# Kernel optimization log

Hardware: AMD Instinct MI355X
Metric: run time of the kernel (lower is better)

Reference implementation:

```python
import jax, jax.numpy as jnp
import numpy as np

DEGREE = 3
NUM_KNOTS = 64
NUM_NEURONS = 256
BATCH = 4096


def _extended_knots():
    """Replicates knots_distribution + sklearn SplineTransformer knot extension.

    Base knots (nk-2 values): linspace(-0.002,-0.001,dg) ++ linspace(0,1,nk-2*dg-2)
    ++ linspace(1.001,1.002,dg). sklearn then pads `degree` knots on each side
    using the boundary knot spacing, giving M = nk - 2 + 2*degree knots and
    M - degree - 1 = nk + degree - 3 = nk basis functions (degree==3).
    """
    dg, nk = DEGREE, NUM_KNOTS
    base = np.concatenate([
        np.linspace(-0.002, -0.001, dg),
        np.linspace(0.0, 1.0, nk - 2 * dg - 2),
        np.linspace(1.001, 1.002, dg),
    ])
    dist_lo = base[1] - base[0]
    dist_hi = base[-1] - base[-2]
    left = base[0] - dist_lo * np.arange(dg, 0, -1)
    right = base[-1] + dist_hi * np.arange(1, dg + 1)
    return jnp.asarray(np.concatenate([left, base, right]), dtype=jnp.float32)


def _bspline_basis(x, t, degree):
    """Vectorized Cox-de Boor recursion.

    x: (..., ) samples; t: (M,) extended knots.
    Returns basis of shape (..., M - degree - 1).
    """
    xe = x[..., None]
    # order-0: indicator of half-open knot intervals, shape (..., M-1)
    B = ((t[:-1] <= xe) & (xe < t[1:])).astype(x.dtype)
    for k in range(1, degree + 1):
        d1 = t[k:-1] - t[:-k - 1]   # (M-k-1,)
        d2 = t[k + 1:] - t[1:-k]    # (M-k-1,)
        w1 = jnp.where(d1 != 0, (xe - t[:-k - 1]) / jnp.where(d1 != 0, d1, 1.0), 0.0)
        w2 = jnp.where(d2 != 0, (t[k + 1:] - xe) / jnp.where(d2 != 0, d2, 1.0), 0.0)
        B = w1 * B[..., :-1] + w2 * B[..., 1:]
    return B


def setup_inputs() -> dict:
    key = jax.random.key(0)
    k1, k2, k3 = jax.random.split(key, 3)
    x = jax.random.uniform(k1, (BATCH, NUM_NEURONS), dtype=jnp.float32)
    control_p = jax.random.normal(k2, (NUM_KNOTS, NUM_NEURONS), dtype=jnp.float32)
    bias = jax.random.normal(k3, (NUM_NEURONS,), dtype=jnp.float32)
    return {"x": x, "control_p": control_p, "bias": bias}


def reference(x, control_p, bias):
    t = _extended_knots()
    # Same B-spline knot vector for every feature, so compute basis jointly:
    # basis[b, f, k] == (torch) basises.permute(1,2,0)[b, k, f]
    basis = _bspline_basis(x, t, DEGREE)          # (batch, F, num_knots)
    out = jnp.einsum('bfk,kf->bf', basis, control_p) + bias
    return out
```

## Files before the change

### kernel.cpp

```cpp
#include <hip/hip_runtime.h>

#define NF 256
#define NT 68

__device__ __forceinline__ float knotf(int idx) {
    if (idx <= 5) return -0.0035f + 0.0005f * (float)idx;
    if (idx >= 62) return 1.001f + 0.0005f * (float)(idx - 62);
    int j = idx - 6;
    if (j == 55) return 1.0f;
    return (float)((double)j * (1.0 / 55.0));
}

__global__ __launch_bounds__(256) void bspline_kernel(
    const float* __restrict__ x,
    const float* __restrict__ cp,
    const float* __restrict__ bias,
    float* __restrict__ out,
    int total4)
{
    __shared__ float t[NT];
    __shared__ float rd11[61], rd21[61], rd22[61], rd31[61], rd32[61], rd33[61];

    const int tid = threadIdx.x;
    if (tid < NT) t[tid] = knotf(tid);
    __syncthreads();
    if (tid >= 6 && tid <= 60) {
        rd11[tid] = 1.0f / (t[tid + 1] - t[tid]);
        rd21[tid] = 1.0f / (t[tid + 1] - t[tid - 1]);
        rd22[tid] = 1.0f / (t[tid + 2] - t[tid]);
        rd31[tid] = 1.0f / (t[tid + 1] - t[tid - 2]);
        rd32[tid] = 1.0f / (t[tid + 2] - t[tid - 1]);
        rd33[tid] = 1.0f / (t[tid + 3] - t[tid]);
    }
    __syncthreads();

    const int gid = blockIdx.x * blockDim.x + tid;
    if (gid >= total4) return;

    const float4 xv = reinterpret_cast<const float4*>(x)[gid];
    const int f0 = (gid * 4) & (NF - 1);
    const float4 bv = reinterpret_cast<const float4*>(bias)[f0 >> 2];

    float xs[4] = {xv.x, xv.y, xv.z, xv.w};
    float rs[4];

#pragma unroll
    for (int l = 0; l < 4; ++l) {
        const float xx = xs[l];
        int j = (int)(xx * 55.0f);
        j = j < 0 ? 0 : (j > 54 ? 54 : j);
        int i = j + 6;
        if (i > 6 && xx < t[i]) --i;
        else if (i < 60 && xx >= t[i + 1]) ++i;

        const float l1 = xx - t[i];
        const float r1 = t[i + 1] - xx;
        const float l2 = xx - t[i - 1];
        const float r2 = t[i + 2] - xx;
        const float l3 = xx - t[i - 2];
        const float r3 = t[i + 3] - xx;

        float temp = rd11[i];
        float N0 = r1 * temp;
        float N1 = l1 * temp;
        temp = N0 * rd21[i];
        N0 = r1 * temp;
        float saved = l2 * temp;
        temp = N1 * rd22[i];
        N1 = saved + r2 * temp;
        float N2 = l1 * temp;
        temp = N0 * rd31[i];
        N0 = r1 * temp;
        saved = l3 * temp;
        temp = N1 * rd32[i];
        N1 = saved + r2 * temp;
        saved = l2 * temp;
        temp = N2 * rd33[i];
        N2 = saved + r3 * temp;
        const float N3 = l1 * temp;

        const float* c = cp + (i - 3) * NF + f0 + l;
        rs[l] = N0 * c[0] + N1 * c[NF] + N2 * c[2 * NF] + N3 * c[3 * NF];
    }

    float4 ov;
    ov.x = rs[0] + bv.x;
    ov.y = rs[1] + bv.y;
    ov.z = rs[2] + bv.z;
    ov.w = rs[3] + bv.w;
    reinterpret_cast<float4*>(out)[gid] = ov;
}

extern "C" void kernel_launch(void* const* d_in, const int* in_sizes, int n_in,
                              void* d_out, int out_size, void* d_ws, size_t ws_size,
                              hipStream_t stream) {
    const float* x    = (const float*)d_in[0];
    const float* cp   = (const float*)d_in[1];
    const float* bias = (const float*)d_in[2];
    float* out = (float*)d_out;

    const int total4 = out_size / 4;
    const int block = 256;
    const int grid = (total4 + block - 1) / block;
    bspline_kernel<<<grid, block, 0, stream>>>(x, cp, bias, out, total4);
}
```

Measured before the change: 66.79 us.

## Stage control points in LDS and compute knots analytically per thread

Each block now copies the whole 64x256 control-point table into shared memory and processes 8 batch rows, one feature per thread. The gathers then read from LDS instead of scattered global memory. Knot positions and their reciprocal spans are computed in closed form with hardware rcp, replacing the shared-memory knot tables and the interval correction step. The trade-offs are a 64KB per-block copy that repeats across 512 blocks, lower occupancy from the large LDS footprint, possible small differences near knot boundaries, and an assumption that the batch divides by 8.

```diff
diff --git a/kernel.cpp b/kernel.cpp
--- a/kernel.cpp
+++ b/kernel.cpp
@@ -1,94 +1,77 @@
 #include <hip/hip_runtime.h>
 
 #define NF 256
-#define NT 68
+#define NK 64
+#define ROWS_PER_BLOCK 8
 
-__device__ __forceinline__ float knotf(int idx) {
-    if (idx <= 5) return -0.0035f + 0.0005f * (float)idx;
-    if (idx >= 62) return 1.001f + 0.0005f * (float)(idx - 62);
-    int j = idx - 6;
-    if (j == 55) return 1.0f;
-    return (float)((double)j * (1.0 / 55.0));
-}
 
-__global__ __launch_bounds__(256) void bspline_kernel(
+__global__ __launch_bounds__(256, 2) void bspline_kernel(
     const float* __restrict__ x,
     const float* __restrict__ cp,
     const float* __restrict__ bias,
-    float* __restrict__ out,
-    int total4)
+    float* __restrict__ out)
 {
-    __shared__ float t[NT];
-    __shared__ float rd11[61], rd21[61], rd22[61], rd31[61], rd32[61], rd33[61];
+    __shared__ float4 cpl4[NK * NF / 4];
+    float* cpl = reinterpret_cast<float*>(cpl4);
 
     const int tid = threadIdx.x;
-    if (tid < NT) t[tid] = knotf(tid);
-    __syncthreads();
-    if (tid >= 6 && tid <= 60) {
-        rd11[tid] = 1.0f / (t[tid + 1] - t[tid]);
-        rd21[tid] = 1.0f / (t[tid + 1] - t[tid - 1]);
-        rd22[tid] = 1.0f / (t[tid + 2] - t[tid]);
-        rd31[tid] = 1.0f / (t[tid + 1] - t[tid - 2]);
-        rd32[tid] = 1.0f / (t[tid + 2] - t[tid - 1]);
-        rd33[tid] = 1.0f / (t[tid + 3] - t[tid]);
+
+    {
+        const float4* cp4 = reinterpret_cast<const float4*>(cp);
+#pragma unroll
+        for (int it = 0; it < NK * NF / 4 / 256; ++it)
+            cpl4[tid + 256 * it] = cp4[tid + 256 * it];
     }
+
+    const float bv = bias[tid];
     __syncthreads();
 
-    const int gid = blockIdx.x * blockDim.x + tid;
-    if (gid >= total4) return;
-
-    const float4 xv = reinterpret_cast<const float4*>(x)[gid];
-    const int f0 = (gid * 4) & (NF - 1);
-    const float4 bv = reinterpret_cast<const float4*>(bias)[f0 >> 2];
-
-    float xs[4] = {xv.x, xv.y, xv.z, xv.w};
-    float rs[4];
+    const int r0 = blockIdx.x * ROWS_PER_BLOCK;
+    constexpr float inv55 = 1.0f / 55.0f;
 
 #pragma unroll
-    for (int l = 0; l < 4; ++l) {
-        const float xx = xs[l];
-        int j = (int)(xx * 55.0f);
-        j = j < 0 ? 0 : (j > 54 ? 54 : j);
-        int i = j + 6;
-        if (i > 6 && xx < t[i]) --i;
-        else if (i < 60 && xx >= t[i + 1]) ++i;
+    for (int j = 0; j < ROWS_PER_BLOCK; ++j) {
+        const float xx = x[(r0 + j) * NF + tid];
 
-        const float l1 = xx - t[i];
-        const float r1 = t[i + 1] - xx;
-        const float l2 = xx - t[i - 1];
-        const float r2 = t[i + 2] - xx;
-        const float l3 = xx - t[i - 2];
-        const float r3 = t[i + 3] - xx;
+        float jf = floorf(xx * 55.0f);
+        jf = fminf(fmaxf(jf, 0.0f), 54.0f);
+        const int ji = (int)jf;
 
-        float temp = rd11[i];
+        const float t_im2 = fmaxf(fmaf(jf, 5e-4f, -1.5e-3f), (jf - 2.0f) * inv55);
+        const float t_im1 = fmaxf(fmaf(jf, 5e-4f, -1.0e-3f), (jf - 1.0f) * inv55);
+        const float t_i   = jf * inv55;
+        const float t_ip1 = (jf + 1.0f) * inv55;
+        const float t_ip2 = fminf((jf + 2.0f) * inv55, fmaf(jf, 5e-4f, 0.974f));
+        const float t_ip3 = fminf((jf + 3.0f) * inv55, fmaf(jf, 5e-4f, 0.9745f));
+
+        const float l1 = xx - t_i,   r1 = t_ip1 - xx;
+        const float l2 = xx - t_im1, r2 = t_ip2 - xx;
+        const float l3 = xx - t_im2, r3 = t_ip3 - xx;
+
+        const float rd11 = __builtin_amdgcn_rcpf(l1 + r1);
+        const float rd21 = __builtin_amdgcn_rcpf(l2 + r1);
+        const float rd22 = __builtin_amdgcn_rcpf(l1 + r2);
+        const float rd31 = __builtin_amdgcn_rcpf(l3 + r1);
+        const float rd32 = __builtin_amdgcn_rcpf(l2 + r2);
+        const float rd33 = __builtin_amdgcn_rcpf(l1 + r3);
+
+        float temp = rd11;
         float N0 = r1 * temp;
         float N1 = l1 * temp;
-        temp = N0 * rd21[i];
-        N0 = r1 * temp;
-        float saved = l2 * temp;
-        temp = N1 * rd22[i];
-        N1 = saved + r2 * temp;
-        float N2 = l1 * temp;
-        temp = N0 * rd31[i];
-        N0 = r1 * temp;
-        saved = l3 * temp;
-        temp = N1 * rd32[i];
-        N1 = saved + r2 * temp;
-        saved = l2 * temp;
-        temp = N2 * rd33[i];
-        N2 = saved + r3 * temp;
-        const float N3 = l1 * temp;
+        temp = N0 * rd21; N0 = r1 * temp; float saved = l2 * temp;
+        temp = N1 * rd22; N1 = fmaf(r2, temp, saved); float N2 = l1 * temp;
+        temp = N0 * rd31; N0 = r1 * temp; saved = l3 * temp;
+        temp = N1 * rd32; N1 = fmaf(r2, temp, saved); saved = l2 * temp;
+        temp = N2 * rd33; N2 = fmaf(r3, temp, saved); const float N3 = l1 * temp;
 
-        const float* c = cp + (i - 3) * NF + f0 + l;
-        rs[l] = N0 * c[0] + N1 * c[NF] + N2 * c[2 * NF] + N3 * c[3 * NF];
+        const float* c = &cpl[(ji + 3) * NF + tid];
+        float acc = fmaf(N0, c[0 * NF], bv);
+        acc = fmaf(N1, c[1 * NF], acc);
+        acc = fmaf(N2, c[2 * NF], acc);
+        acc = fmaf(N3, c[3 * NF], acc);
+
+        out[(r0 + j) * NF + tid] = acc;
     }
-
-    float4 ov;
-    ov.x = rs[0] + bv.x;
-    ov.y = rs[1] + bv.y;
-    ov.z = rs[2] + bv.z;
-    ov.w = rs[3] + bv.w;
-    reinterpret_cast<float4*>(out)[gid] = ov;
 }
 
 extern "C" void kernel_launch(void* const* d_in, const int* in_sizes, int n_in,
@@ -99,8 +82,7 @@
     const float* bias = (const float*)d_in[2];
     float* out = (float*)d_out;
 
-    const int total4 = out_size / 4;
-    const int block = 256;
-    const int grid = (total4 + block - 1) / block;
-    bspline_kernel<<<grid, block, 0, stream>>>(x, cp, bias, out, total4);
+    const int batch = in_sizes[0] / NF;
+    const int grid = batch / ROWS_PER_BLOCK;
+    bspline_kernel<<<grid, 256, 0, stream>>>(x, cp, bias, out);
 }
```

New measurement: 60.97 us. 8.7% less time.
